# Kernel optimization log

Measured on AMD Instinct MI355X. Metric: run time of the kernel, lower is better.

## Reference

```python
import jax, jax.numpy as jnp
import numpy as np

X_SCALE, X_ZP = 0.03, -66      # int8 quant params (qmin=-128, qmax=127)
Y_SCALE, Y_ZP = 0.025, 160     # uint8 quant params (qmin=0, qmax=255)
M = K = N = 4096


def setup_inputs() -> dict:
    key = jax.random.key(0)
    kx, ky = jax.random.split(key)
    # x holds int8-range values [-128, 127], y holds uint8-range values [0, 255]
    x = jax.random.randint(kx, (M, K), -128, 128, dtype=jnp.int32)
    y = jax.random.randint(ky, (K, N), 0, 256, dtype=jnp.int32)
    return {"x": x, "y": y}


def reference(x, y):
    # dequantize_per_tensor: (q - zero_point) * scale  (values already in [qmin, qmax])
    xf = (x.astype(jnp.float32) - X_ZP) * X_SCALE   # [M, K]
    yf = (y.astype(jnp.float32) - Y_ZP) * Y_SCALE   # [K, N]
    return jnp.matmul(xf, yf)                       # [M, N]
```

## Files before the change

kernel.cpp:

```cpp
#include <hip/hip_runtime.h>
#include <stdint.h>

#define Mdim 4096
#define Kdim 4096
#define Ndim 4096

typedef __attribute__((ext_vector_type(4))) int v4i;
typedef __attribute__((ext_vector_type(16))) int v16i;

__device__ __forceinline__ void gload_lds16(const void* g, void* l) {
  __builtin_amdgcn_global_load_lds(
      (__attribute__((address_space(1))) void*)(uintptr_t)g,
      (__attribute__((address_space(3))) void*)(uint32_t)(uintptr_t)l,
      16, 0, 0);
}

__global__ __launch_bounds__(256) void pack_x_kernel(const int* __restrict__ x,
                                                     char* __restrict__ x8,
                                                     int* __restrict__ rsx) {
  const int row = blockIdx.x;
  const int t = threadIdx.x;
  const int4* src = (const int4*)(x + (size_t)row * Kdim);
  int* dst = (int*)(x8 + (size_t)row * Kdim);
  int sum = 0;
#pragma unroll
  for (int i = 0; i < 4; ++i) {
    int4 v = src[t + 256 * i];
    sum += v.x + v.y + v.z + v.w;
    dst[t + 256 * i] =
        (v.x & 0xff) | ((v.y & 0xff) << 8) | ((v.z & 0xff) << 16) | (v.w << 24);
  }
#pragma unroll
  for (int o = 32; o > 0; o >>= 1) sum += __shfl_down(sum, o, 64);
  __shared__ int red[4];
  if ((t & 63) == 0) red[t >> 6] = sum;
  __syncthreads();
  if (t == 0) rsx[row] = red[0] + red[1] + red[2] + red[3];
}

__global__ __launch_bounds__(256) void pack_yt_kernel(const int* __restrict__ y,
                                                      char* __restrict__ yt,
                                                      int* __restrict__ csy) {
  __shared__ int wt[64 * 17];
  const int t = threadIdx.x;
  const int n0 = blockIdx.x * 64;
  const int k0 = blockIdx.y * 64;
  const int c = t & 15;
  const int r0 = t >> 4;
#pragma unroll
  for (int s = 0; s < 4; ++s) {
    const int r = r0 + s * 16;
    int4 v = *(const int4*)(y + (size_t)(k0 + r) * Ndim + n0 + c * 4);
    v.x -= 128; v.y -= 128; v.z -= 128; v.w -= 128;
    wt[r * 17 + c] =
        (v.x & 0xff) | ((v.y & 0xff) << 8) | ((v.z & 0xff) << 16) | (v.w << 24);
  }
  __syncthreads();
  const int n = t >> 2;
  const int kq = t & 3;
  const int colw = n >> 2;
  const int byi = (n & 3) * 8;
  int outw[4];
  int bsum = 0;
#pragma unroll
  for (int j = 0; j < 4; ++j) {
    int b[4];
#pragma unroll
    for (int jj = 0; jj < 4; ++jj) {
      const int word = wt[(kq * 16 + j * 4 + jj) * 17 + colw];
      b[jj] = (word >> byi) & 0xff;
      bsum += (int)(char)b[jj];
    }
    outw[j] = b[0] | (b[1] << 8) | (b[2] << 16) | (b[3] << 24);
  }
  *(int4*)(yt + (size_t)(n0 + n) * Kdim + k0 + kq * 16) =
      make_int4(outw[0], outw[1], outw[2], outw[3]);
  bsum += __shfl_xor(bsum, 1, 64);
  bsum += __shfl_xor(bsum, 2, 64);
  if (kq == 0) atomicAdd(csy + n0 + n, bsum);
}

__global__ __launch_bounds__(512, 2) void gemm_i8_kernel(
    const char* __restrict__ A, const char* __restrict__ B,
    const int* __restrict__ rsx, const int* __restrict__ csy,
    float* __restrict__ out) {
  __shared__ __align__(16) char lds[2 * 32768];
  const int t = threadIdx.x;
  const int l = t & 63;
  const int w = t >> 6;
  const int warow = w >> 1;
  const int wbcol = w & 1;
  const int bm = blockIdx.y * 256;
  const int bn = blockIdx.x * 256;

  v16i acc[2][4];
#pragma unroll
  for (int i = 0; i < 2; ++i)
#pragma unroll
    for (int j = 0; j < 4; ++j)
#pragma unroll
      for (int q = 0; q < 16; ++q) acc[i][j][q] = 0;

  const int srow = t >> 2;
  const int cswz = ((t & 3) ^ ((t >> 3) & 3)) * 16;
  const char* gA = A + (size_t)(bm + srow) * Kdim + cswz;
  const char* gB = B + (size_t)(bn + srow) * Kdim + cswz;

#define STAGE(buf_off, koff)                                                  \
  do {                                                                        \
    _Pragma("unroll") for (int i = 0; i < 2; ++i)                             \
        gload_lds16(gA + (koff) + (size_t)i * 128 * Kdim,                     \
                    lds + (buf_off) + i * 8192 + t * 16);                     \
    _Pragma("unroll") for (int i = 0; i < 2; ++i)                             \
        gload_lds16(gB + (koff) + (size_t)i * 128 * Kdim,                     \
                    lds + (buf_off) + 16384 + i * 8192 + t * 16);             \
  } while (0)

  const int arow = warow * 64 + (l & 31);
  const int brow = wbcol * 128 + (l & 31);
  const int lhalf = l >> 5;
  const int lkey = (l >> 1) & 3;

#define COMPUTE(buf_off)                                                      \
  do {                                                                        \
    const char* As = lds + (buf_off);                                         \
    const char* Bs = lds + (buf_off) + 16384;                                 \
    _Pragma("unroll") for (int ks = 0; ks < 2; ++ks) {                        \
      const int slot = ((ks * 2 + lhalf) ^ lkey) * 16;                        \
      v4i a[2], b[4];                                                         \
      _Pragma("unroll") for (int i = 0; i < 2; ++i)                           \
          a[i] = *(const v4i*)(As + (arow + i * 32) * 64 + slot);             \
      _Pragma("unroll") for (int j = 0; j < 4; ++j)                           \
          b[j] = *(const v4i*)(Bs + (brow + j * 32) * 64 + slot);             \
      _Pragma("unroll") for (int i = 0; i < 2; ++i)                           \
          _Pragma("unroll") for (int j = 0; j < 4; ++j)                       \
              acc[i][j] = __builtin_amdgcn_mfma_i32_32x32x32_i8(              \
                  a[i], b[j], acc[i][j], 0, 0, 0);                            \
    }                                                                         \
  } while (0)

  STAGE(0, 0);
  __syncthreads();
  for (int kt = 0; kt < 64; kt += 2) {
    if (kt + 1 < 64) STAGE(32768, (kt + 1) * 64);
    COMPUTE(0);
    __syncthreads();
    if (kt + 2 < 64) STAGE(0, (kt + 2) * 64);
    COMPUTE(32768);
    __syncthreads();
  }

  const int col = l & 31;
#pragma unroll
  for (int i = 0; i < 2; ++i) {
    const int gm0 = bm + warow * 64 + i * 32;
#pragma unroll
    for (int j = 0; j < 4; ++j) {
      const int gn = bn + wbcol * 128 + j * 32 + col;
      const int cs = 66 * csy[gn] - 8650752;
#pragma unroll
      for (int r = 0; r < 16; ++r) {
        const int row = (r & 3) + 8 * (r >> 2) + 4 * lhalf;
        const int gm = gm0 + row;
        const int val = acc[i][j][r] - 32 * rsx[gm] + cs;
        out[(size_t)gm * Ndim + gn] = 7.5e-4f * (float)val;
      }
    }
  }
#undef STAGE
#undef COMPUTE
}

extern "C" void kernel_launch(void* const* d_in, const int* in_sizes, int n_in,
                              void* d_out, int out_size, void* d_ws, size_t ws_size,
                              hipStream_t stream) {
  (void)in_sizes; (void)n_in; (void)out_size; (void)ws_size;
  const int* x = (const int*)d_in[0];
  const int* y = (const int*)d_in[1];
  float* out = (float*)d_out;
  char* ws = (char*)d_ws;
  char* x8 = ws;
  char* yt = ws + (size_t)Mdim * Kdim;
  int* rsx = (int*)(ws + (size_t)Mdim * Kdim + (size_t)Kdim * Ndim);
  int* csy = rsx + Mdim;

  hipMemsetAsync(csy, 0, Ndim * sizeof(int), stream);
  pack_x_kernel<<<Mdim, 256, 0, stream>>>(x, x8, rsx);
  pack_yt_kernel<<<dim3(Ndim / 64, Kdim / 64), 256, 0, stream>>>(y, yt, csy);
  gemm_i8_kernel<<<dim3(Ndim / 256, Mdim / 256), 512, 0, stream>>>(x8, yt, rsx, csy, out);
}
```

Measured before the change: 241.9 us.

## Triple-buffer LDS with fine-grained vmcnt waits and MFMA priority boost

Moves the int8 GEMM main loop from double to triple buffering in LDS, so two K-tiles of global-to-LDS loads are in flight while one is computed. Full __syncthreads is replaced with raw barriers plus explicit s_waitcnt vmcnt counts, so each wave waits only for the oldest stage. s_setprio is raised around the MFMA block. LDS grows to 96KB per block, which may break the requested two blocks per CU occupancy.

```diff
diff --git a/kernel.cpp b/kernel.cpp
--- a/kernel.cpp
+++ b/kernel.cpp
@@ -84,7 +84,7 @@
     const char* __restrict__ A, const char* __restrict__ B,
     const int* __restrict__ rsx, const int* __restrict__ csy,
     float* __restrict__ out) {
-  __shared__ __align__(16) char lds[2 * 32768];
+  __shared__ __align__(16) char lds[3 * 32768];
   const int t = threadIdx.x;
   const int l = t & 63;
   const int w = t >> 6;
@@ -125,6 +125,7 @@
   do {                                                                        \
     const char* As = lds + (buf_off);                                         \
     const char* Bs = lds + (buf_off) + 16384;                                 \
+    __builtin_amdgcn_s_setprio(1);                                            \
     _Pragma("unroll") for (int ks = 0; ks < 2; ++ks) {                        \
       const int slot = ((ks * 2 + lhalf) ^ lkey) * 16;                        \
       v4i a[2], b[4];                                                         \
@@ -137,18 +138,55 @@
               acc[i][j] = __builtin_amdgcn_mfma_i32_32x32x32_i8(              \
                   a[i], b[j], acc[i][j], 0, 0, 0);                            \
     }                                                                         \
+    __builtin_amdgcn_s_setprio(0);                                            \
   } while (0)
 
+#define BAR()                                                                 \
+  do {                                                                        \
+    asm volatile("" ::: "memory");                                            \
+    __builtin_amdgcn_s_barrier();                                             \
+    asm volatile("" ::: "memory");                                            \
+  } while (0)
+#define WAITV(n) asm volatile("s_waitcnt vmcnt(" #n ")" ::: "memory")
+
   STAGE(0, 0);
-  __syncthreads();
-  for (int kt = 0; kt < 64; kt += 2) {
-    if (kt + 1 < 64) STAGE(32768, (kt + 1) * 64);
+  STAGE(32768, 1 * 64);
+  STAGE(65536, 2 * 64);
+  WAITV(8);
+  BAR();
+
+#pragma unroll 1
+  for (int kt = 0; kt < 60; kt += 3) {
     COMPUTE(0);
-    __syncthreads();
-    if (kt + 2 < 64) STAGE(0, (kt + 2) * 64);
+    BAR();
+    STAGE(0, (kt + 3) * 64);
+    WAITV(8);
+    BAR();
     COMPUTE(32768);
-    __syncthreads();
-  }
+    BAR();
+    STAGE(32768, (kt + 4) * 64);
+    WAITV(8);
+    BAR();
+    COMPUTE(65536);
+    BAR();
+    STAGE(65536, (kt + 5) * 64);
+    WAITV(8);
+    BAR();
+  }
+  COMPUTE(0);
+  BAR();
+  STAGE(0, 63 * 64);
+  WAITV(8);
+  BAR();
+  COMPUTE(32768);
+  BAR();
+  WAITV(4);
+  BAR();
+  COMPUTE(65536);
+  BAR();
+  WAITV(0);
+  BAR();
+  COMPUTE(0);
 
   const int col = l & 31;
 #pragma unroll
@@ -169,6 +207,8 @@
   }
 #undef STAGE
 #undef COMPUTE
+#undef BAR
+#undef WAITV
 }
 
 extern "C" void kernel_launch(void* const* d_in, const int* in_sizes, int n_in,
```

Result: no change. 243.4 us (+0.6%).

## Triple-buffer LDS and interleave async staging with MFMA phases using barriers and setprio

Applied to the files above, without the earlier changes.

Replaces the double-buffered K loop with a three-buffer LDS ring in which the next-next tile is prefetched. Each tile is split into four MFMA groups, and one global-to-LDS load is issued per group. Workgroup barriers, sched_barrier fences, s_setprio and explicit vmcnt waits are placed around each group to keep the matrix cores fed while loads are in flight. The cost is a 96KB LDS footprint, which may cut the number of blocks resident per CU, plus many more barriers per tile.

```diff
diff --git a/kernel.cpp b/kernel.cpp
--- a/kernel.cpp
+++ b/kernel.cpp
@@ -84,7 +84,7 @@
     const char* __restrict__ A, const char* __restrict__ B,
     const int* __restrict__ rsx, const int* __restrict__ csy,
     float* __restrict__ out) {
-  __shared__ __align__(16) char lds[2 * 32768];
+  __shared__ __align__(16) char lds[3 * 32768];
   const int t = threadIdx.x;
   const int l = t & 63;
   const int w = t >> 6;
@@ -116,39 +116,116 @@
                     lds + (buf_off) + 16384 + i * 8192 + t * 16);             \
   } while (0)
 
+#define STG(sbo, koff, idx)                                                   \
+  gload_lds16(((idx) < 2 ? gA : gB) + (koff) + (size_t)((idx)&1) * 128 * Kdim,\
+              lds + (sbo) + ((idx) < 2 ? 0 : 16384) + ((idx)&1) * 8192 +      \
+                  t * 16)
+
   const int arow = warow * 64 + (l & 31);
   const int brow = wbcol * 128 + (l & 31);
   const int lhalf = l >> 5;
   const int lkey = (l >> 1) & 3;
-
-#define COMPUTE(buf_off)                                                      \
+  const int slot0 = ((0 + lhalf) ^ lkey) * 16;
+  const int slot1 = ((2 + lhalf) ^ lkey) * 16;
+
+#define MFMA(a, b, c) __builtin_amdgcn_mfma_i32_32x32x32_i8(a, b, c, 0, 0, 0)
+#define SETP(n) __builtin_amdgcn_s_setprio(n)
+#define FENCE() __builtin_amdgcn_sched_barrier(0)
+#define BAR()                                                                 \
   do {                                                                        \
-    const char* As = lds + (buf_off);                                         \
-    const char* Bs = lds + (buf_off) + 16384;                                 \
-    _Pragma("unroll") for (int ks = 0; ks < 2; ++ks) {                        \
-      const int slot = ((ks * 2 + lhalf) ^ lkey) * 16;                        \
-      v4i a[2], b[4];                                                         \
-      _Pragma("unroll") for (int i = 0; i < 2; ++i)                           \
-          a[i] = *(const v4i*)(As + (arow + i * 32) * 64 + slot);             \
-      _Pragma("unroll") for (int j = 0; j < 4; ++j)                           \
-          b[j] = *(const v4i*)(Bs + (brow + j * 32) * 64 + slot);             \
-      _Pragma("unroll") for (int i = 0; i < 2; ++i)                           \
-          _Pragma("unroll") for (int j = 0; j < 4; ++j)                       \
-              acc[i][j] = __builtin_amdgcn_mfma_i32_32x32x32_i8(              \
-                  a[i], b[j], acc[i][j], 0, 0, 0);                            \
+    asm volatile("" ::: "memory");                                            \
+    __builtin_amdgcn_s_barrier();                                             \
+    asm volatile("" ::: "memory");                                            \
+  } while (0)
+#define WAITV(n) asm volatile("s_waitcnt vmcnt(" #n ")" ::: "memory")
+
+#define TILE(bo, sbo, skoff, dostage, TAILWAIT)                               \
+  do {                                                                        \
+    const char* As = lds + (bo);                                              \
+    const char* Bs = lds + (bo) + 16384;                                      \
+    v4i a0, a1, b0, b1;                                                       \
+                        \
+    a0 = *(const v4i*)(As + arow * 64 + slot0);                               \
+    a1 = *(const v4i*)(As + (arow + 32) * 64 + slot0);                        \
+    b0 = *(const v4i*)(Bs + brow * 64 + slot0);                               \
+    b1 = *(const v4i*)(Bs + (brow + 32) * 64 + slot0);                        \
+    if (dostage) STG(sbo, skoff, 0);                                          \
+    BAR();                                                                    \
+    FENCE();                                                                  \
+    SETP(1);                                                                  \
+    acc[0][0] = MFMA(a0, b0, acc[0][0]);                                      \
+    acc[0][1] = MFMA(a0, b1, acc[0][1]);                                      \
+    acc[1][0] = MFMA(a1, b0, acc[1][0]);                                      \
+    acc[1][1] = MFMA(a1, b1, acc[1][1]);                                      \
+    SETP(0);                                                                  \
+    FENCE();                                                                  \
+    BAR();                                                                    \
+                              \
+    {                                                                         \
+      v4i b2 = *(const v4i*)(Bs + (brow + 64) * 64 + slot0);                  \
+      v4i b3 = *(const v4i*)(Bs + (brow + 96) * 64 + slot0);                  \
+      if (dostage) STG(sbo, skoff, 1);                                        \
+      BAR();                                                                  \
+      FENCE();                                                                \
+      SETP(1);                                                                \
+      acc[0][2] = MFMA(a0, b2, acc[0][2]);                                    \
+      acc[0][3] = MFMA(a0, b3, acc[0][3]);                                    \
+      acc[1][2] = MFMA(a1, b2, acc[1][2]);                                    \
+      acc[1][3] = MFMA(a1, b3, acc[1][3]);                                    \
+      SETP(0);                                                                \
+      FENCE();                                                                \
+      BAR();                                                                  \
+    }                                                                         \
+                                        \
+    a0 = *(const v4i*)(As + arow * 64 + slot1);                               \
+    a1 = *(const v4i*)(As + (arow + 32) * 64 + slot1);                        \
+    b0 = *(const v4i*)(Bs + brow * 64 + slot1);                               \
+    b1 = *(const v4i*)(Bs + (brow + 32) * 64 + slot1);                        \
+    if (dostage) STG(sbo, skoff, 2);                                          \
+    BAR();                                                                    \
+    FENCE();                                                                  \
+    SETP(1);                                                                  \
+    acc[0][0] = MFMA(a0, b0, acc[0][0]);                                      \
+    acc[0][1] = MFMA(a0, b1, acc[0][1]);                                      \
+    acc[1][0] = MFMA(a1, b0, acc[1][0]);                                      \
+    acc[1][1] = MFMA(a1, b1, acc[1][1]);                                      \
+    SETP(0);                                                                  \
+    FENCE();                                                                  \
+    BAR();                                                                    \
+                   \
+    {                                                                         \
+      v4i b2 = *(const v4i*)(Bs + (brow + 64) * 64 + slot1);                  \
+      v4i b3 = *(const v4i*)(Bs + (brow + 96) * 64 + slot1);                  \
+      if (dostage) STG(sbo, skoff, 3);                                        \
+      BAR();                                                                  \
+      FENCE();                                                                \
+      SETP(1);                                                                \
+      acc[0][2] = MFMA(a0, b2, acc[0][2]);                                    \
+      acc[0][3] = MFMA(a0, b3, acc[0][3]);                                    \
+      acc[1][2] = MFMA(a1, b2, acc[1][2]);                                    \
+      acc[1][3] = MFMA(a1, b3, acc[1][3]);                                    \
+      SETP(0);                                                                \
+      FENCE();                                                                \
+      TAILWAIT;                                                               \
+      BAR();                                                                  \
     }                                                                         \
   } while (0)
 
   STAGE(0, 0);
-  __syncthreads();
-  for (int kt = 0; kt < 64; kt += 2) {
-    if (kt + 1 < 64) STAGE(32768, (kt + 1) * 64);
-    COMPUTE(0);
-    __syncthreads();
-    if (kt + 2 < 64) STAGE(0, (kt + 2) * 64);
-    COMPUTE(32768);
-    __syncthreads();
-  }
+  STAGE(32768, 64);
+  WAITV(4);
+  BAR();
+
+#pragma unroll 1
+  for (int kt = 0; kt < 60; kt += 3) {
+    TILE(0, 65536, (kt + 2) * 64, 1, WAITV(4));
+    TILE(32768, 0, (kt + 3) * 64, 1, WAITV(4));
+    TILE(65536, 32768, (kt + 4) * 64, 1, WAITV(4));
+  }
+  TILE(0, 65536, 62 * 64, 1, WAITV(4));
+  TILE(32768, 0, 63 * 64, 1, WAITV(4));
+  TILE(65536, 0, 0, 0, WAITV(0));
+  TILE(0, 0, 0, 0, (void)0);
 
   const int col = l & 31;
 #pragma unroll
@@ -168,7 +245,13 @@
     }
   }
 #undef STAGE
-#undef COMPUTE
+#undef STG
+#undef TILE
+#undef MFMA
+#undef SETP
+#undef FENCE
+#undef BAR
+#undef WAITV
 }
 
 extern "C" void kernel_launch(void* const* d_in, const int* in_sizes, int n_in,
```

Measured after the change: 238.9 us. No clear change (-1.2%).

## Deepen int8 GEMM pipeline to four LDS stages with register-prefetched fragments

Applied to the files above, without the earlier changes.

Replaces the two-buffer LDS loop in the int8 GEMM with a four-slot LDS ring and two register sets for the A/B fragments. Each step reads the next tile's fragments from LDS and issues global-to-LDS loads three tiles ahead, then runs the MFMAs on the previous fragments. Explicit vmcnt waits replace the full syncs, and s_setprio and sched_barrier keep the issue order. The goal is to hide global-load latency and LDS reads behind the MFMAs. In exchange it uses 128 KB of LDS per block and more VGPRs, which rules out two resident blocks per CU, and the hand-written wait counts add correctness risk.

```diff
diff --git a/kernel.cpp b/kernel.cpp
--- a/kernel.cpp
+++ b/kernel.cpp
@@ -84,7 +84,7 @@
     const char* __restrict__ A, const char* __restrict__ B,
     const int* __restrict__ rsx, const int* __restrict__ csy,
     float* __restrict__ out) {
-  __shared__ __align__(16) char lds[2 * 32768];
+  __shared__ __align__(16) char lds[4 * 32768];
   const int t = threadIdx.x;
   const int l = t & 63;
   const int w = t >> 6;
@@ -106,7 +106,7 @@
   const char* gA = A + (size_t)(bm + srow) * Kdim + cswz;
   const char* gB = B + (size_t)(bn + srow) * Kdim + cswz;
 
-#define STAGE(buf_off, koff)                                                  \
+#define STG4(buf_off, koff)                                                   \
   do {                                                                        \
     _Pragma("unroll") for (int i = 0; i < 2; ++i)                             \
         gload_lds16(gA + (koff) + (size_t)i * 128 * Kdim,                     \
@@ -120,35 +120,83 @@
   const int brow = wbcol * 128 + (l & 31);
   const int lhalf = l >> 5;
   const int lkey = (l >> 1) & 3;
-
-#define COMPUTE(buf_off)                                                      \
-  do {                                                                        \
-    const char* As = lds + (buf_off);                                         \
-    const char* Bs = lds + (buf_off) + 16384;                                 \
-    _Pragma("unroll") for (int ks = 0; ks < 2; ++ks) {                        \
-      const int slot = ((ks * 2 + lhalf) ^ lkey) * 16;                        \
-      v4i a[2], b[4];                                                         \
-      _Pragma("unroll") for (int i = 0; i < 2; ++i)                           \
-          a[i] = *(const v4i*)(As + (arow + i * 32) * 64 + slot);             \
-      _Pragma("unroll") for (int j = 0; j < 4; ++j)                           \
-          b[j] = *(const v4i*)(Bs + (brow + j * 32) * 64 + slot);             \
-      _Pragma("unroll") for (int i = 0; i < 2; ++i)                           \
-          _Pragma("unroll") for (int j = 0; j < 4; ++j)                       \
-              acc[i][j] = __builtin_amdgcn_mfma_i32_32x32x32_i8(              \
-                  a[i], b[j], acc[i][j], 0, 0, 0);                            \
+  const int slot0 = ((0 + lhalf) ^ lkey) * 16;
+  const int slot1 = ((2 + lhalf) ^ lkey) * 16;
+
+  v4i fa[2][2][2];
+  v4i fb[2][2][4];
+
+#define READF(BK, RBO)                                                        \
+  do {                                                                        \
+    const char* As_ = lds + (RBO);                                            \
+    const char* Bs_ = lds + (RBO) + 16384;                                    \
+    _Pragma("unroll") for (int i = 0; i < 2; ++i) {                           \
+      fa[BK][0][i] = *(const v4i*)(As_ + (arow + i * 32) * 64 + slot0);       \
+      fa[BK][1][i] = *(const v4i*)(As_ + (arow + i * 32) * 64 + slot1);       \
     }                                                                         \
-  } while (0)
-
-  STAGE(0, 0);
-  __syncthreads();
-  for (int kt = 0; kt < 64; kt += 2) {
-    if (kt + 1 < 64) STAGE(32768, (kt + 1) * 64);
-    COMPUTE(0);
-    __syncthreads();
-    if (kt + 2 < 64) STAGE(0, (kt + 2) * 64);
-    COMPUTE(32768);
-    __syncthreads();
-  }
+    _Pragma("unroll") for (int j = 0; j < 4; ++j) {                           \
+      fb[BK][0][j] = *(const v4i*)(Bs_ + (brow + j * 32) * 64 + slot0);       \
+      fb[BK][1][j] = *(const v4i*)(Bs_ + (brow + j * 32) * 64 + slot1);       \
+    }                                                                         \
+  } while (0)
+
+#define MFMA(a, b, c) __builtin_amdgcn_mfma_i32_32x32x32_i8(a, b, c, 0, 0, 0)
+#define SETP(n) __builtin_amdgcn_s_setprio(n)
+#define FENCE() __builtin_amdgcn_sched_barrier(0)
+#define BAR()                                                                 \
+  do {                                                                        \
+    asm volatile("" ::: "memory");                                            \
+    __builtin_amdgcn_s_barrier();                                             \
+    asm volatile("" ::: "memory");                                            \
+  } while (0)
+#define WAITV(n) asm volatile("s_waitcnt vmcnt(" #n ")" ::: "memory")
+
+#define DOMFMA(BK)                                                            \
+  do {                                                                        \
+    SETP(1);                                                                  \
+    _Pragma("unroll") for (int ks = 0; ks < 2; ++ks)                          \
+        _Pragma("unroll") for (int i = 0; i < 2; ++i)                         \
+            _Pragma("unroll") for (int j = 0; j < 4; ++j)                     \
+                acc[i][j] = MFMA(fa[BK][ks][i], fb[BK][ks][j], acc[i][j]);    \
+    SETP(0);                                                                  \
+  } while (0)
+
+#define TILEX(RBK, RBO, SBO, SKOFF, MBK)                                      \
+  do {                                                                        \
+    READF(RBK, RBO);                                                          \
+    STG4(SBO, SKOFF);                                                         \
+    FENCE();                                                                  \
+    DOMFMA(MBK);                                                              \
+    WAITV(4);                                                                 \
+    BAR();                                                                    \
+  } while (0)
+
+  STG4(0, 0);
+  STG4(32768, 64);
+  STG4(65536, 128);
+  WAITV(8);
+  BAR();
+  READF(0, 0);
+  WAITV(4);
+  BAR();
+
+#pragma unroll 1
+  for (int kt = 0; kt < 60; kt += 4) {
+    TILEX(1, 32768, 98304, (kt + 3) * 64, 0);
+    TILEX(0, 65536, 0, (kt + 4) * 64, 1);
+    TILEX(1, 98304, 32768, (kt + 5) * 64, 0);
+    TILEX(0, 0, 65536, (kt + 6) * 64, 1);
+  }
+  TILEX(1, 32768, 98304, 63 * 64, 0);
+  READF(0, 65536);
+  FENCE();
+  DOMFMA(1);
+  WAITV(0);
+  BAR();
+  READF(1, 98304);
+  FENCE();
+  DOMFMA(0);
+  DOMFMA(1);
 
   const int col = l & 31;
 #pragma unroll
@@ -167,8 +215,15 @@
       }
     }
   }
-#undef STAGE
-#undef COMPUTE
+#undef STG4
+#undef READF
+#undef TILEX
+#undef DOMFMA
+#undef MFMA
+#undef SETP
+#undef FENCE
+#undef BAR
+#undef WAITV
 }
 
 extern "C" void kernel_launch(void* const* d_in, const int* in_sizes, int n_in,
```

Result: no change. 242.3 us (+0.1%).
